# Optimization experiments

Hardware: AMD Instinct MI355X
Metric: run time of the kernel (lower is better)

The kernel has to match this reference:

```python
import jax, jax.numpy as jnp
import numpy as np

N_NODES = 50000
N_EDGES = 800000
N_FEAT = 128
HIDDEN = 256
BN_EPS = 1e-5


def setup_inputs() -> dict:
    key = jax.random.key(0)
    ks = jax.random.split(key, 8)
    x = jax.random.normal(ks[0], (N_NODES, N_FEAT), dtype=jnp.float32)
    edge_index = jax.random.randint(ks[1], (2, N_EDGES), 0, N_NODES, dtype=jnp.int64)
    # Xavier-uniform linear weights (as in weights_init), zero biases
    def xavier(k, fan_in, fan_out):
        lim = float(np.sqrt(6.0 / (fan_in + fan_out)))
        return jax.random.uniform(k, (fan_in, fan_out), jnp.float32, -lim, lim)
    return {
        "x": x,
        "edge_index": edge_index,
        "W1": xavier(ks[2], N_FEAT, HIDDEN),
        "b1": jnp.zeros((HIDDEN,), jnp.float32),
        "g1": jnp.ones((HIDDEN,), jnp.float32),
        "be1": jnp.zeros((HIDDEN,), jnp.float32),
        "W2": xavier(ks[3], HIDDEN, HIDDEN),
        "b2": jnp.zeros((HIDDEN,), jnp.float32),
        "g2": jnp.ones((HIDDEN,), jnp.float32),
        "be2": jnp.zeros((HIDDEN,), jnp.float32),
        "Wfc": xavier(ks[4], HIDDEN, HIDDEN),
        "bfc": jnp.zeros((HIDDEN,), jnp.float32),
    }


def gcn_conv(x, src, dst, deg_inv_sqrt, W, b):
    """PyG GCNConv: out_i = sum_{j->i} d_i^-1/2 d_j^-1/2 (x_j W) + b,
    with self-loops already appended to (src, dst)."""
    h = x @ W                                        # [N, out]
    norm = deg_inv_sqrt[src] * deg_inv_sqrt[dst]     # [E+N]
    msgs = h[src] * norm[:, None]                    # gather + scale
    out = jax.ops.segment_sum(msgs, dst, num_segments=x.shape[0])
    return out + b


def batch_norm(x, gamma, beta):
    # training-mode BatchNorm1d: batch stats over nodes, biased variance
    mean = jnp.mean(x, axis=0)
    var = jnp.mean(jnp.square(x - mean), axis=0)
    return (x - mean) * jax.lax.rsqrt(var + BN_EPS) * gamma + beta


def reference(x, edge_index, W1, b1, g1, be1, W2, b2, g2, be2, Wfc, bfc):
    n = x.shape[0]
    loop = jnp.arange(n, dtype=edge_index.dtype)
    src = jnp.concatenate([edge_index[0], loop])
    dst = jnp.concatenate([edge_index[1], loop])
    deg = jax.ops.segment_sum(jnp.ones_like(src, dtype=x.dtype), dst, num_segments=n)
    deg_inv_sqrt = jnp.where(deg > 0, jax.lax.rsqrt(jnp.maximum(deg, 1.0)), 0.0)

    h = gcn_conv(x, src, dst, deg_inv_sqrt, W1, b1)
    h = batch_norm(h, g1, be1)
    # dropout is identity in deterministic (eval) reference
    h = gcn_conv(h, src, dst, deg_inv_sqrt, W2, b2)
    h = batch_norm(h, g2, be2)
    return h @ Wfc + bfc
```

## Files before the change

### kernel.cpp

```cpp
#include <hip/hip_runtime.h>
#include <hip/hip_bf16.h>

#define NFEAT 128
#define HID 256
#define BN_EPS 1e-5f
#define NBIN 64

typedef __attribute__((ext_vector_type(8))) __bf16 bf16x8;
typedef __attribute__((ext_vector_type(4))) float f32x4;

static __device__ __forceinline__ float bflo(unsigned u) {
    union { unsigned x; float f; } c; c.x = u << 16; return c.f;
}
static __device__ __forceinline__ float bfhi(unsigned u) {
    union { unsigned x; float f; } c; c.x = u & 0xffff0000u; return c.f;
}

__global__ void k_count(const int* __restrict__ ei, int E, int* __restrict__ cnt,
                        int* __restrict__ rank) {
    int e = blockIdx.x * blockDim.x + threadIdx.x;
    if (e < E) rank[e] = atomicAdd(&cnt[ei[E + e]], 1);
}

__global__ void k_scan1(const int* __restrict__ cnt, int n, int* __restrict__ partial,
                        int* __restrict__ blk_total) {
    __shared__ int sh[256];
    int i = blockIdx.x * 256 + threadIdx.x;
    int v = (i < n) ? cnt[i] : 0;
    sh[threadIdx.x] = v;
    __syncthreads();
    for (int off = 1; off < 256; off <<= 1) {
        int x = (threadIdx.x >= off) ? sh[threadIdx.x - off] : 0;
        __syncthreads();
        sh[threadIdx.x] += x;
        __syncthreads();
    }
    if (i < n) partial[i] = sh[threadIdx.x] - v;
    if (threadIdx.x == 255) blk_total[blockIdx.x] = sh[255];
}

__global__ void k_finalize(const int* __restrict__ partial, const int* __restrict__ blk_total,
                           const int* __restrict__ cnt, int n, int nblk,
                           int* __restrict__ row_start, float* __restrict__ dinv) {
    __shared__ int sw[4];
    const int t = threadIdx.x;
    const int b = blockIdx.x;
    int v = (t < b && t < nblk) ? blk_total[t] : 0;
#pragma unroll
    for (int m = 1; m < 64; m <<= 1) v += __shfl_xor(v, m);
    if ((t & 63) == 0) sw[t >> 6] = v;
    __syncthreads();
    int pref = sw[0] + sw[1] + sw[2] + sw[3];
    int i = b * 256 + t;
    if (i < n) {
        row_start[i] = partial[i] + pref;
        dinv[i] = rsqrtf((float)(cnt[i] + 1));
    }
}

__global__ void k_fillcast(int fillBlocks, int castBlocks, const int* __restrict__ ei,
                           const int* __restrict__ rank, const int* __restrict__ row_start,
                           int E, int* __restrict__ col, const float* __restrict__ x,
                           const float* __restrict__ dinv, __hip_bfloat16* __restrict__ xs,
                           int n4, const float* __restrict__ W1,
                           __hip_bfloat16* __restrict__ Wt1) {
    const int bid = blockIdx.x;
    const int t = threadIdx.x;
    if (bid < fillBlocks) {
        int e = bid * 256 + t;
        if (e < E) {
            int d = ei[E + e];
            col[row_start[d] + rank[e]] = ei[e];
        }
    } else if (bid < fillBlocks + castBlocks) {
        int i = (bid - fillBlocks) * 256 + t;
        if (i < n4) {
            float d = dinv[i >> 5];
            float4 v = *(const float4*)(x + (size_t)i * 4);
            __hip_bfloat16* o = xs + (size_t)i * 4;
            o[0] = __float2bfloat16(v.x * d);
            o[1] = __float2bfloat16(v.y * d);
            o[2] = __float2bfloat16(v.z * d);
            o[3] = __float2bfloat16(v.w * d);
        }
    } else {
        int idx = (bid - fillBlocks - castBlocks) * 256 + t;
        int nn = idx & 255;
        int k = idx >> 8;
        Wt1[nn * 128 + k] = __float2bfloat16(W1[k * 256 + nn]);
    }
}

__global__ __launch_bounds__(256) void k_bnfoldW(const float* __restrict__ gs,
                                                 const float* __restrict__ g,
                                                 const float* __restrict__ be,
                                                 const float* __restrict__ b, float invN,
                                                 const float* __restrict__ W1,
                                                 const float* __restrict__ W2,
                                                 __hip_bfloat16* __restrict__ WfT,
                                                 float* __restrict__ uvec) {
    __shared__ float shs[256], shb[256];
    const int c = threadIdx.x;
    float s = 0.f, q = 0.f;
    for (int r = 0; r < NBIN; r++) {
        s += gs[r * 512 + c];
        q += gs[r * 512 + 256 + c];
    }
    float mean = s * invN;
    float var = q * invN - mean * mean;
    float scl = rsqrtf(var + BN_EPS) * g[c];
    shs[c] = scl;
    shb[c] = (b[c] - mean) * scl + be[c];
    __syncthreads();
    if (blockIdx.x < 128) {
        int k = blockIdx.x;
        float acc = 0.f;
        for (int m = 0; m < 256; m++) acc += W1[k * 256 + m] * shs[m] * W2[m * 256 + c];
        WfT[(size_t)c * 128 + k] = __float2bfloat16(acc);
    } else {
        float acc = 0.f;
        for (int m = 0; m < 256; m++) acc += W2[m * 256 + c] * shb[m];
        uvec[c] = acc;
    }
}

__global__ __launch_bounds__(256) void k_fold2(const float* __restrict__ gs,
                                               const float* __restrict__ g,
                                               const float* __restrict__ be, float invN,
                                               const float* __restrict__ Wfc,
                                               const float* __restrict__ bfc,
                                               __hip_bfloat16* __restrict__ Wtf,
                                               float* __restrict__ bias2) {
    __shared__ float shs[256], sho[256];
    const int c = threadIdx.x;
    float s = 0.f, q = 0.f;
    for (int r = 0; r < NBIN; r++) {
        s += gs[r * 512 + c];
        q += gs[r * 512 + 256 + c];
    }
    float mean = s * invN;
    float var = q * invN - mean * mean;
    float scl = rsqrtf(var + BN_EPS) * g[c];
    shs[c] = scl;
    sho[c] = (0.f - mean) * scl + be[c];
    __syncthreads();
    if (blockIdx.x < 256) {
        int k = blockIdx.x;
        Wtf[(size_t)c * 256 + k] = __float2bfloat16(Wfc[k * 256 + c] * shs[k]);
    } else {
        float acc = bfc[c];
        for (int m = 0; m < 256; m++) acc += sho[m] * Wfc[m * 256 + c];
        bias2[c] = acc;
    }
}

template <bool SCALE>
__global__ __launch_bounds__(256) void k_spmm(const __hip_bfloat16* __restrict__ Hs,
                                              const int* __restrict__ rs,
                                              const int* __restrict__ rc,
                                              const int* __restrict__ col,
                                              const float* __restrict__ dinv,
                                              __hip_bfloat16* __restrict__ out,
                                              float* __restrict__ rv, int N) {
    const int wid = blockIdx.x * 4 + (threadIdx.x >> 6);
    if (wid >= N) return;
    const int lane = threadIdx.x & 63;
    const int ch = lane * 2;
    const int s = rs[wid];
    const int deg = rc[wid];
    const float di = dinv[wid];

    unsigned u0 = *(const unsigned*)(Hs + (size_t)wid * 128 + ch);
    float a0, a1, dsum = 0.f;
    if constexpr (SCALE) { a0 = di * bflo(u0); a1 = di * bfhi(u0); }
    else { a0 = bflo(u0); a1 = bfhi(u0); }

    int e = 0;
    for (; e + 8 <= deg; e += 8) {
        int idx[8];
#pragma unroll
        for (int j = 0; j < 8; j++) idx[j] = col[s + e + j];
        float dj[8];
#pragma unroll
        for (int j = 0; j < 8; j++) dj[j] = dinv[idx[j]];
        unsigned u[8];
#pragma unroll
        for (int j = 0; j < 8; j++) u[j] = *(const unsigned*)(Hs + (size_t)idx[j] * 128 + ch);
#pragma unroll
        for (int j = 0; j < 8; j++) {
            if constexpr (SCALE) { a0 += dj[j] * bflo(u[j]); a1 += dj[j] * bfhi(u[j]); }
            else { a0 += bflo(u[j]); a1 += bfhi(u[j]); dsum += dj[j]; }
        }
    }
    for (; e < deg; e++) {
        int i0 = col[s + e];
        float d0 = dinv[i0];
        unsigned uu = *(const unsigned*)(Hs + (size_t)i0 * 128 + ch);
        if constexpr (SCALE) { a0 += d0 * bflo(uu); a1 += d0 * bfhi(uu); }
        else { a0 += bflo(uu); a1 += bfhi(uu); dsum += d0; }
    }
    union { unsigned w; unsigned short us[2]; } o;
    __hip_bfloat16 b0 = __float2bfloat16(di * a0); o.us[0] = *(unsigned short*)&b0;
    __hip_bfloat16 b1 = __float2bfloat16(di * a1); o.us[1] = *(unsigned short*)&b1;
    *(unsigned*)(out + (size_t)wid * 128 + ch) = o.w;
    if (!SCALE && rv && lane == 0) rv[wid] = di * (di + dsum);
}

template <int K, bool STATS>
__global__ __launch_bounds__(256, 4) void k_gemm2(const __hip_bfloat16* __restrict__ A,
                                                  const __hip_bfloat16* __restrict__ Bt,
                                                  const float* __restrict__ bias,
                                                  __hip_bfloat16* __restrict__ outb,
                                                  float* __restrict__ outf,
                                                  float* __restrict__ gs,
                                                  const float* __restrict__ rvec,
                                                  const float* __restrict__ uvec, int M) {
    constexpr int NC = K / 64;
    constexpr int LDR = 72;
    __shared__ __align__(16) unsigned short Bs[2 * 128 * LDR];
    float* sred = (float*)Bs;
    float* qred = sred + 512;

    const int t = threadIdx.x;
    const int wv = t >> 6;
    const int lane = t & 63;
    const int mlane = lane & 15;
    const int quad = lane >> 4;
    const int m0 = blockIdx.x * 128;
    const int n0 = blockIdx.y * 128;
    const int arow0 = m0 + wv * 32 + mlane;

    auto stage = [&](int c, int buf) {
#pragma unroll
        for (int i = 0; i < 4; i++) {
            int idx = t + i * 256;
            int row = idx >> 3;
            int c4 = idx & 7;
            uint4 v = *(const uint4*)(Bt + (size_t)(n0 + row) * K + c * 64 + c4 * 8);
            *(uint4*)(Bs + buf * (128 * LDR) + row * LDR + c4 * 8) = v;
        }
    };
    auto loadA = [&](int c, bf16x8 (&dst)[2][2]) {
#pragma unroll
        for (int mt = 0; mt < 2; mt++)
#pragma unroll
            for (int ks = 0; ks < 2; ks++)
                dst[mt][ks] = *(const bf16x8*)(A + (size_t)(arow0 + mt * 16) * K + c * 64 +
                                               ks * 32 + quad * 8);
    };

    f32x4 acc[2][8];
#pragma unroll
    for (int mt = 0; mt < 2; mt++)
#pragma unroll
        for (int i = 0; i < 8; i++) acc[mt][i] = (f32x4){0.f, 0.f, 0.f, 0.f};

    bf16x8 aP[2][2], aQ[2][2];
    loadA(0, aP);
    stage(0, 0);

    auto mmachunk = [&](int c, bf16x8 (&ac)[2][2]) {
        const unsigned short* base = Bs + (c & 1) * (128 * LDR);
#pragma unroll
        for (int nt = 0; nt < 8; nt++) {
            const unsigned short* bp = base + (nt * 16 + mlane) * LDR + quad * 8;
#pragma unroll
            for (int ks = 0; ks < 2; ks++) {
                bf16x8 b = *(const bf16x8*)(bp + ks * 32);
                acc[0][nt] = __builtin_amdgcn_mfma_f32_16x16x32_bf16(ac[0][ks], b, acc[0][nt], 0, 0, 0);
                acc[1][nt] = __builtin_amdgcn_mfma_f32_16x16x32_bf16(ac[1][ks], b, acc[1][nt], 0, 0, 0);
            }
        }
    };

#pragma unroll
    for (int c = 0; c < NC; c++) {
        __syncthreads();
        if (c + 1 < NC) {
            stage(c + 1, (c + 1) & 1);
            if ((c & 1) == 0) loadA(c + 1, aQ); else loadA(c + 1, aP);
        }
        if ((c & 1) == 0) mmachunk(c, aP); else mmachunk(c, aQ);
    }

    float rv[2][4] = {{0.f, 0.f, 0.f, 0.f}, {0.f, 0.f, 0.f, 0.f}};
    if (rvec) {
#pragma unroll
        for (int mt = 0; mt < 2; mt++)
#pragma unroll
            for (int r = 0; r < 4; r++) {
                int row = m0 + wv * 32 + mt * 16 + quad * 4 + r;
                if (row < M) rv[mt][r] = rvec[row];
            }
    }
    float sp[8], qp[8];
#pragma unroll
    for (int nt = 0; nt < 8; nt++) {
        int colx = n0 + nt * 16 + mlane;
        float bv = bias[colx];
        float uvn = uvec ? uvec[colx] : 0.f;
        float s = 0.f, q = 0.f;
#pragma unroll
        for (int mt = 0; mt < 2; mt++)
#pragma unroll
            for (int r = 0; r < 4; r++) {
                int row = m0 + wv * 32 + mt * 16 + quad * 4 + r;
                if (row < M) {
                    float h = acc[mt][nt][r] + bv + rv[mt][r] * uvn;
                    if (outb) outb[(size_t)row * HID + colx] = __float2bfloat16(h);
                    if (outf) outf[(size_t)row * HID + colx] = h;
                    s += h;
                    q += h * h;
                }
            }
        sp[nt] = s;
        qp[nt] = q;
    }
    if constexpr (STATS) {
#pragma unroll
        for (int nt = 0; nt < 8; nt++) {
            sp[nt] += __shfl_xor(sp[nt], 16);
            sp[nt] += __shfl_xor(sp[nt], 32);
            qp[nt] += __shfl_xor(qp[nt], 16);
            qp[nt] += __shfl_xor(qp[nt], 32);
        }
        __syncthreads();
        if (quad == 0) {
#pragma unroll
            for (int nt = 0; nt < 8; nt++) {
                sred[wv * 128 + nt * 16 + mlane] = sp[nt];
                qred[wv * 128 + nt * 16 + mlane] = qp[nt];
            }
        }
        __syncthreads();
        if (t < 128) {
            float ss = sred[t] + sred[128 + t] + sred[256 + t] + sred[384 + t];
            float qq = qred[t] + qred[128 + t] + qred[256 + t] + qred[384 + t];
            float* bin = gs + (blockIdx.x & (NBIN - 1)) * 512;
            atomicAdd(&bin[n0 + t], ss);
            atomicAdd(&bin[256 + n0 + t], qq);
        }
    }
}

extern "C" void kernel_launch(void* const* d_in, const int* in_sizes, int n_in, void* d_out,
                              int out_size, void* d_ws, size_t ws_size, hipStream_t stream) {
    const float* x = (const float*)d_in[0];
    const int* ei = (const int*)d_in[1];
    const float* W1 = (const float*)d_in[2];
    const float* b1 = (const float*)d_in[3];
    const float* g1 = (const float*)d_in[4];
    const float* be1 = (const float*)d_in[5];
    const float* W2 = (const float*)d_in[6];
    const float* b2 = (const float*)d_in[7];
    const float* g2 = (const float*)d_in[8];
    const float* be2 = (const float*)d_in[9];
    const float* Wfc = (const float*)d_in[10];
    const float* bfc = (const float*)d_in[11];
    float* out = (float*)d_out;

    const int N = in_sizes[0] / NFEAT;
    const int E = in_sizes[1] / 2;
    const float invN = 1.0f / (float)N;

    char* ws = (char*)d_ws;
    size_t off = 0;
    auto alloc = [&](size_t bytes) -> void* {
        void* p = ws + off;
        off += (bytes + 255) & ~(size_t)255;
        return p;
    };
    int* row_cnt = (int*)alloc((size_t)N * 4);
    float* gs1 = (float*)alloc((size_t)NBIN * 512 * 4);
    float* gs2 = (float*)alloc((size_t)NBIN * 512 * 4);
    size_t zero_bytes = off;
    int* partial = (int*)alloc((size_t)N * 4);
    int* row_start = (int*)alloc((size_t)N * 4);
    int* blk = (int*)alloc(256 * 4);
    float* dinv = (float*)alloc((size_t)N * 4);
    int* rank = (int*)alloc((size_t)E * 4);
    int* col_idx = (int*)alloc((size_t)E * 4);
    float* uvec = (float*)alloc(256 * 4);
    float* bias2 = (float*)alloc(256 * 4);
    float* rvec = (float*)alloc((size_t)(N + 128) * 4);
    __hip_bfloat16* Wt1 = (__hip_bfloat16*)alloc(256 * 128 * 2);
    __hip_bfloat16* Wtf = (__hip_bfloat16*)alloc(256 * 256 * 2);
    __hip_bfloat16* WfT = (__hip_bfloat16*)alloc(256 * 128 * 2);
    __hip_bfloat16* xs = (__hip_bfloat16*)alloc((size_t)(N + 128) * NFEAT * 2);
    __hip_bfloat16* aggX = (__hip_bfloat16*)alloc((size_t)(N + 128) * NFEAT * 2);
    __hip_bfloat16* h2 = (__hip_bfloat16*)alloc((size_t)(N + 128) * HID * 2);
    __hip_bfloat16* t2 = xs;

    hipMemsetAsync(row_cnt, 0, zero_bytes, stream);

    const int nblk = (N + 255) / 256;
    const int fillBlocks = (E + 255) / 256;
    const int castBlocks = (N * NFEAT / 4 + 255) / 256;

    k_count<<<fillBlocks, 256, 0, stream>>>(ei, E, row_cnt, rank);
    k_scan1<<<nblk, 256, 0, stream>>>(row_cnt, N, partial, blk);
    k_finalize<<<nblk, 256, 0, stream>>>(partial, blk, row_cnt, N, nblk, row_start, dinv);
    k_fillcast<<<fillBlocks + castBlocks + 128, 256, 0, stream>>>(
        fillBlocks, castBlocks, ei, rank, row_start, E, col_idx, x, dinv, xs,
        N * NFEAT / 4, W1, Wt1);

    const int sg = (N + 3) / 4;
    dim3 gg((N + 127) / 128, 2);

    k_spmm<false><<<sg, 256, 0, stream>>>(xs, row_start, row_cnt, col_idx, dinv, aggX, rvec, N);
    k_spmm<true><<<sg, 256, 0, stream>>>(aggX, row_start, row_cnt, col_idx, dinv, t2, nullptr, N);
    k_gemm2<NFEAT, true><<<gg, 256, 0, stream>>>(aggX, Wt1, b1, nullptr, nullptr, gs1,
                                                 nullptr, nullptr, N);
    k_bnfoldW<<<129, 256, 0, stream>>>(gs1, g1, be1, b1, invN, W1, W2, WfT, uvec);
    k_gemm2<NFEAT, true><<<gg, 256, 0, stream>>>(t2, WfT, b2, h2, nullptr, gs2, rvec, uvec, N);
    k_fold2<<<257, 256, 0, stream>>>(gs2, g2, be2, invN, Wfc, bfc, Wtf, bias2);
    k_gemm2<HID, false><<<gg, 256, 0, stream>>>(h2, Wtf, bias2, nullptr, out, nullptr,
                                                nullptr, nullptr, N);
}
```

Before: 314.3 us.

## Compute BatchNorm statistics via Gram matrices and fold all layers into one GEMM

Instead of running per-layer GEMMs that materialize hidden activations just to collect BatchNorm mean and variance, the code now builds 128x128 Gram matrices and column sums of the aggregated inputs. It derives the BN statistics analytically from these through the weight matrices. Both BN layers and the final linear layer are then folded into a single 128-to-256 weight, so only one large GEMM over nodes remains. This removes two full-size GEMMs and the bf16 hidden buffer. In exchange it adds several small reduction kernels, and the E[h^2]-mean^2 variance computed from bf16 Gram sums may lose precision.

```diff
diff --git a/kernel.cpp b/kernel.cpp
--- a/kernel.cpp
+++ b/kernel.cpp
@@ -4,7 +4,9 @@
 #define NFEAT 128
 #define HID 256
 #define BN_EPS 1e-5f
-#define NBIN 64
+#define GR 64
+#define GLDW 72
+#define GB 128
 
 typedef __attribute__((ext_vector_type(8))) __bf16 bf16x8;
 typedef __attribute__((ext_vector_type(4))) float f32x4;
@@ -58,12 +60,11 @@
     }
 }
 
-__global__ void k_fillcast(int fillBlocks, int castBlocks, const int* __restrict__ ei,
+__global__ void k_fillcast(int fillBlocks, const int* __restrict__ ei,
                            const int* __restrict__ rank, const int* __restrict__ row_start,
                            int E, int* __restrict__ col, const float* __restrict__ x,
                            const float* __restrict__ dinv, __hip_bfloat16* __restrict__ xs,
-                           int n4, const float* __restrict__ W1,
-                           __hip_bfloat16* __restrict__ Wt1) {
+                           int n4) {
     const int bid = blockIdx.x;
     const int t = threadIdx.x;
     if (bid < fillBlocks) {
@@ -72,7 +73,7 @@
             int d = ei[E + e];
             col[row_start[d] + rank[e]] = ei[e];
         }
-    } else if (bid < fillBlocks + castBlocks) {
+    } else {
         int i = (bid - fillBlocks) * 256 + t;
         if (i < n4) {
             float d = dinv[i >> 5];
@@ -83,74 +84,6 @@
             o[2] = __float2bfloat16(v.z * d);
             o[3] = __float2bfloat16(v.w * d);
         }
-    } else {
-        int idx = (bid - fillBlocks - castBlocks) * 256 + t;
-        int nn = idx & 255;
-        int k = idx >> 8;
-        Wt1[nn * 128 + k] = __float2bfloat16(W1[k * 256 + nn]);
-    }
-}
-
-__global__ __launch_bounds__(256) void k_bnfoldW(const float* __restrict__ gs,
-                                                 const float* __restrict__ g,
-                                                 const float* __restrict__ be,
-                                                 const float* __restrict__ b, float invN,
-                                                 const float* __restrict__ W1,
-                                                 const float* __restrict__ W2,
-                                                 __hip_bfloat16* __restrict__ WfT,
-                                                 float* __restrict__ uvec) {
-    __shared__ float shs[256], shb[256];
-    const int c = threadIdx.x;
-    float s = 0.f, q = 0.f;
-    for (int r = 0; r < NBIN; r++) {
-        s += gs[r * 512 + c];
-        q += gs[r * 512 + 256 + c];
-    }
-    float mean = s * invN;
-    float var = q * invN - mean * mean;
-    float scl = rsqrtf(var + BN_EPS) * g[c];
-    shs[c] = scl;
-    shb[c] = (b[c] - mean) * scl + be[c];
-    __syncthreads();
-    if (blockIdx.x < 128) {
-        int k = blockIdx.x;
-        float acc = 0.f;
-        for (int m = 0; m < 256; m++) acc += W1[k * 256 + m] * shs[m] * W2[m * 256 + c];
-        WfT[(size_t)c * 128 + k] = __float2bfloat16(acc);
-    } else {
-        float acc = 0.f;
-        for (int m = 0; m < 256; m++) acc += W2[m * 256 + c] * shb[m];
-        uvec[c] = acc;
-    }
-}
-
-__global__ __launch_bounds__(256) void k_fold2(const float* __restrict__ gs,
-                                               const float* __restrict__ g,
-                                               const float* __restrict__ be, float invN,
-                                               const float* __restrict__ Wfc,
-                                               const float* __restrict__ bfc,
-                                               __hip_bfloat16* __restrict__ Wtf,
-                                               float* __restrict__ bias2) {
-    __shared__ float shs[256], sho[256];
-    const int c = threadIdx.x;
-    float s = 0.f, q = 0.f;
-    for (int r = 0; r < NBIN; r++) {
-        s += gs[r * 512 + c];
-        q += gs[r * 512 + 256 + c];
-    }
-    float mean = s * invN;
-    float var = q * invN - mean * mean;
-    float scl = rsqrtf(var + BN_EPS) * g[c];
-    shs[c] = scl;
-    sho[c] = (0.f - mean) * scl + be[c];
-    __syncthreads();
-    if (blockIdx.x < 256) {
-        int k = blockIdx.x;
-        Wtf[(size_t)c * 256 + k] = __float2bfloat16(Wfc[k * 256 + c] * shs[k]);
-    } else {
-        float acc = bfc[c];
-        for (int m = 0; m < 256; m++) acc += sho[m] * Wfc[m * 256 + c];
-        bias2[c] = acc;
     }
 }
 
@@ -206,20 +139,289 @@
     if (!SCALE && rv && lane == 0) rv[wid] = di * (di + dsum);
 }
 
-template <int K, bool STATS>
+__global__ __launch_bounds__(256) void k_gram(const __hip_bfloat16* __restrict__ X1,
+                                              const __hip_bfloat16* __restrict__ X2,
+                                              const float* __restrict__ rvec,
+                                              float* __restrict__ Gp1, float* __restrict__ Gp2,
+                                              float* __restrict__ vp1, float* __restrict__ vp2,
+                                              int N) {
+    __shared__ __align__(16) unsigned short XT[128 * GLDW];
+    __shared__ float sdr[GR];
+    __shared__ float sred[256];
+    const int t = threadIdx.x;
+    const int wv = t >> 6;
+    const int lane = t & 63;
+    const int mlane = lane & 15;
+    const int quad = lane >> 4;
+    const bool r1 = (int)blockIdx.x >= GB;
+    const int bid = r1 ? blockIdx.x - GB : blockIdx.x;
+    const __hip_bfloat16* X = r1 ? X2 : X1;
+    float* Gp = (r1 ? Gp2 : Gp1) + (size_t)bid * 16384;
+    float* vpb = r1 ? (vp2 + (size_t)bid * 260) : (vp1 + (size_t)bid * 128);
+
+    f32x4 acc[2][8];
+#pragma unroll
+    for (int mt = 0; mt < 2; mt++)
+#pragma unroll
+        for (int i = 0; i < 8; i++) acc[mt][i] = (f32x4){0.f, 0.f, 0.f, 0.f};
+    float csum = 0.f, c2s = 0.f, srs = 0.f, sr2s = 0.f;
+
+    const int nc = (N + GR - 1) / GR;
+    for (int chk = bid; chk < nc; chk += GB) {
+        const int row0 = chk * GR;
+        __syncthreads();
+#pragma unroll
+        for (int i = 0; i < 4; i++) {
+            int idx = t + i * 256;
+            int k = idx & (GR - 1);
+            int g = idx >> 6;
+            int row = row0 + k;
+            uint4 v = (row < N) ? *(const uint4*)(X + (size_t)row * 128 + g * 8)
+                                : make_uint4(0u, 0u, 0u, 0u);
+            const unsigned short* pv = (const unsigned short*)&v;
+#pragma unroll
+            for (int c = 0; c < 8; c++) XT[(g * 8 + c) * GLDW + k] = pv[c];
+        }
+        if (r1 && t < GR) {
+            int row = row0 + t;
+            sdr[t] = (row < N) ? rvec[row] : 0.f;
+        }
+        __syncthreads();
+        {
+            int cch = t & 127, h = t >> 7;
+            float cs = 0.f, cc = 0.f;
+#pragma unroll
+            for (int k = 0; k < GR / 2; k++) {
+                int kk = h * (GR / 2) + k;
+                float xv = bflo((unsigned)XT[cch * GLDW + kk]);
+                cs += xv;
+                if (r1) cc += xv * sdr[kk];
+            }
+            csum += cs;
+            c2s += cc;
+            if (r1 && t < GR) { float r = sdr[t]; srs += r; sr2s += r * r; }
+        }
+#pragma unroll
+        for (int ks = 0; ks < 2; ks++) {
+            bf16x8 af[2];
+#pragma unroll
+            for (int mt = 0; mt < 2; mt++)
+                af[mt] = *(const bf16x8*)(XT + (wv * 32 + mt * 16 + mlane) * GLDW +
+                                          ks * 32 + quad * 8);
+#pragma unroll
+            for (int nt = 0; nt < 8; nt++) {
+                bf16x8 bfr = *(const bf16x8*)(XT + (nt * 16 + mlane) * GLDW + ks * 32 + quad * 8);
+                acc[0][nt] = __builtin_amdgcn_mfma_f32_16x16x32_bf16(af[0], bfr, acc[0][nt], 0, 0, 0);
+                acc[1][nt] = __builtin_amdgcn_mfma_f32_16x16x32_bf16(af[1], bfr, acc[1][nt], 0, 0, 0);
+            }
+        }
+    }
+#pragma unroll
+    for (int mt = 0; mt < 2; mt++)
+#pragma unroll
+        for (int nt = 0; nt < 8; nt++)
+#pragma unroll
+            for (int r = 0; r < 4; r++)
+                Gp[(wv * 32 + mt * 16 + quad * 4 + r) * 128 + nt * 16 + mlane] = acc[mt][nt][r];
+    sred[t] = csum;
+    __syncthreads();
+    if (t < 128) vpb[t] = sred[t] + sred[t + 128];
+    if (r1) {
+        __syncthreads();
+        sred[t] = c2s;
+        __syncthreads();
+        if (t < 128) vpb[128 + t] = sred[t] + sred[t + 128];
+        if (t < 64) {
+            float a = srs, b = sr2s;
+#pragma unroll
+            for (int m = 1; m < 64; m <<= 1) { a += __shfl_xor(a, m); b += __shfl_xor(b, m); }
+            if (t == 0) { vpb[256] = a; vpb[257] = b; }
+        }
+    }
+}
+
+__global__ __launch_bounds__(256) void k_gfold(const float* __restrict__ Gp1,
+                                               const float* __restrict__ Gp2,
+                                               const float* __restrict__ vp1,
+                                               const float* __restrict__ vp2,
+                                               float* __restrict__ G1, float* __restrict__ G2,
+                                               float* __restrict__ svec) {
+    const int b = blockIdx.x, t = threadIdx.x;
+    if (b < 64) {
+        int e = b * 256 + t;
+        float s = 0.f;
+        for (int p = 0; p < GB; p++) s += Gp1[(size_t)p * 16384 + e];
+        G1[e] = s;
+    } else if (b < 128) {
+        int e = (b - 64) * 256 + t;
+        float s = 0.f;
+        for (int p = 0; p < GB; p++) s += Gp2[(size_t)p * 16384 + e];
+        G2[e] = s;
+    } else {
+        if (t < 128) {
+            float s = 0.f;
+            for (int p = 0; p < GB; p++) s += vp1[(size_t)p * 128 + t];
+            svec[t] = s;
+        } else {
+            int c = t - 128;
+            float s = 0.f;
+            for (int p = 0; p < GB; p++) s += vp2[(size_t)p * 260 + c];
+            svec[128 + c] = s;
+        }
+        __syncthreads();
+        if (t < 128) {
+            float s = 0.f;
+            for (int p = 0; p < GB; p++) s += vp2[(size_t)p * 260 + 128 + t];
+            svec[256 + t] = s;
+        } else if (t == 128) {
+            float s = 0.f;
+            for (int p = 0; p < GB; p++) s += vp2[(size_t)p * 260 + 256];
+            svec[384] = s;
+        } else if (t == 129) {
+            float s = 0.f;
+            for (int p = 0; p < GB; p++) s += vp2[(size_t)p * 260 + 257];
+            svec[385] = s;
+        }
+    }
+}
+
+__global__ __launch_bounds__(128) void k_bnstat1(const float* __restrict__ G1,
+                                                 const float* __restrict__ svec,
+                                                 const float* __restrict__ W1,
+                                                 const float* __restrict__ b1,
+                                                 const float* __restrict__ g1,
+                                                 const float* __restrict__ be1, float invN,
+                                                 float fN, float* __restrict__ sc1,
+                                                 float* __restrict__ bv1) {
+    __shared__ float shw[128], s1[128], s2[128];
+    const int c = blockIdx.x, t = threadIdx.x;
+    shw[t] = W1[t * 256 + c];
+    __syncthreads();
+    const float* gr = G1 + t * 128;
+    float v = 0.f;
+    for (int b = 0; b < 128; b++) v += gr[b] * shw[b];
+    s1[t] = v * shw[t];
+    s2[t] = svec[t] * shw[t];
+    __syncthreads();
+    for (int off = 64; off; off >>= 1) {
+        if (t < off) { s1[t] += s1[t + off]; s2[t] += s2[t + off]; }
+        __syncthreads();
+    }
+    if (t == 0) {
+        float bb = b1[c], mdot = s2[0], vdot = s1[0];
+        float mean = (mdot + fN * bb) * invN;
+        float eh2 = (vdot + 2.f * bb * mdot + fN * bb * bb) * invN;
+        float var = eh2 - mean * mean;
+        float s = rsqrtf(var + BN_EPS) * g1[c];
+        sc1[c] = s;
+        bv1[c] = (bb - mean) * s + be1[c];
+    }
+}
+
+__global__ __launch_bounds__(256) void k_bnfoldW(const float* __restrict__ sc1,
+                                                 const float* __restrict__ bv1,
+                                                 const float* __restrict__ W1,
+                                                 const float* __restrict__ W2,
+                                                 __hip_bfloat16* __restrict__ WfT,
+                                                 float* __restrict__ uvec) {
+    __shared__ float shs[256], shb[256];
+    const int c = threadIdx.x;
+    shs[c] = sc1[c];
+    shb[c] = bv1[c];
+    __syncthreads();
+    if (blockIdx.x < 128) {
+        int k = blockIdx.x;
+        float acc = 0.f;
+        for (int m = 0; m < 256; m++) acc += W1[k * 256 + m] * shs[m] * W2[m * 256 + c];
+        WfT[(size_t)c * 128 + k] = __float2bfloat16(acc);
+    } else {
+        float acc = 0.f;
+        for (int m = 0; m < 256; m++) acc += W2[m * 256 + c] * shb[m];
+        uvec[c] = acc;
+    }
+}
+
+__global__ __launch_bounds__(128) void k_bnstat2(const float* __restrict__ G2,
+                                                 const float* __restrict__ svec,
+                                                 const __hip_bfloat16* __restrict__ WfT,
+                                                 const float* __restrict__ uvec,
+                                                 const float* __restrict__ b2,
+                                                 const float* __restrict__ g2,
+                                                 const float* __restrict__ be2, float invN,
+                                                 float fN, float* __restrict__ sc2,
+                                                 float* __restrict__ ofb2) {
+    __shared__ float shw[128], s1[128], s2[128], s3[128];
+    const int c = blockIdx.x, t = threadIdx.x;
+    shw[t] = __bfloat162float(WfT[(size_t)c * 128 + t]);
+    __syncthreads();
+    const float* gr = G2 + t * 128;
+    float v = 0.f;
+    for (int b = 0; b < 128; b++) v += gr[b] * shw[b];
+    s1[t] = v * shw[t];
+    s2[t] = svec[128 + t] * shw[t];
+    s3[t] = svec[256 + t] * shw[t];
+    __syncthreads();
+    for (int off = 64; off; off >>= 1) {
+        if (t < off) { s1[t] += s1[t + off]; s2[t] += s2[t + off]; s3[t] += s3[t + off]; }
+        __syncthreads();
+    }
+    if (t == 0) {
+        float bb = b2[c], u = uvec[c];
+        float vdot = s1[0], mdot = s2[0], cdot = s3[0];
+        float Sr = svec[384], Sr2 = svec[385];
+        float mean = (mdot + Sr * u + fN * bb) * invN;
+        float eh2 = (vdot + 2.f * u * cdot + 2.f * bb * mdot + Sr2 * u * u +
+                     2.f * bb * u * Sr + fN * bb * bb) * invN;
+        float var = eh2 - mean * mean;
+        float s = rsqrtf(var + BN_EPS) * g2[c];
+        sc2[c] = s;
+        ofb2[c] = (bb - mean) * s + be2[c];
+    }
+}
+
+__global__ __launch_bounds__(256) void k_foldbig(const float* __restrict__ sc2,
+                                                 const float* __restrict__ ofb2,
+                                                 const float* __restrict__ uvec,
+                                                 const float* __restrict__ Wfc,
+                                                 const float* __restrict__ bfc,
+                                                 const __hip_bfloat16* __restrict__ WfT,
+                                                 __hip_bfloat16* __restrict__ WbigT,
+                                                 float* __restrict__ vvec,
+                                                 float* __restrict__ cvec) {
+    __shared__ float sh[256];
+    const int t = threadIdx.x;
+    if (blockIdx.x < 256) {
+        int n = blockIdx.x;
+        sh[t] = sc2[t] * Wfc[t * 256 + n];
+        __syncthreads();
+        if (t < 128) {
+            float acc = 0.f;
+            for (int m = 0; m < 256; m++)
+                acc += __bfloat162float(WfT[(size_t)m * 128 + t]) * sh[m];
+            WbigT[(size_t)n * 128 + t] = __float2bfloat16(acc);
+        }
+    } else {
+        float av = 0.f, ac = bfc[t];
+        for (int m = 0; m < 256; m++) {
+            float w = Wfc[m * 256 + t];
+            av += uvec[m] * sc2[m] * w;
+            ac += ofb2[m] * w;
+        }
+        vvec[t] = av;
+        cvec[t] = ac;
+    }
+}
+
+template <int K>
 __global__ __launch_bounds__(256, 4) void k_gemm2(const __hip_bfloat16* __restrict__ A,
                                                   const __hip_bfloat16* __restrict__ Bt,
                                                   const float* __restrict__ bias,
-                                                  __hip_bfloat16* __restrict__ outb,
                                                   float* __restrict__ outf,
-                                                  float* __restrict__ gs,
                                                   const float* __restrict__ rvec,
                                                   const float* __restrict__ uvec, int M) {
     constexpr int NC = K / 64;
     constexpr int LDR = 72;
     __shared__ __align__(16) unsigned short Bs[2 * 128 * LDR];
-    float* sred = (float*)Bs;
-    float* qred = sred + 512;
 
     const int t = threadIdx.x;
     const int wv = t >> 6;
@@ -284,62 +486,25 @@
     }
 
     float rv[2][4] = {{0.f, 0.f, 0.f, 0.f}, {0.f, 0.f, 0.f, 0.f}};
-    if (rvec) {
-#pragma unroll
-        for (int mt = 0; mt < 2; mt++)
-#pragma unroll
-            for (int r = 0; r < 4; r++) {
-                int row = m0 + wv * 32 + mt * 16 + quad * 4 + r;
-                if (row < M) rv[mt][r] = rvec[row];
-            }
-    }
-    float sp[8], qp[8];
+#pragma unroll
+    for (int mt = 0; mt < 2; mt++)
+#pragma unroll
+        for (int r = 0; r < 4; r++) {
+            int row = m0 + wv * 32 + mt * 16 + quad * 4 + r;
+            if (row < M) rv[mt][r] = rvec[row];
+        }
 #pragma unroll
     for (int nt = 0; nt < 8; nt++) {
         int colx = n0 + nt * 16 + mlane;
         float bv = bias[colx];
-        float uvn = uvec ? uvec[colx] : 0.f;
-        float s = 0.f, q = 0.f;
+        float uvn = uvec[colx];
 #pragma unroll
         for (int mt = 0; mt < 2; mt++)
 #pragma unroll
             for (int r = 0; r < 4; r++) {
                 int row = m0 + wv * 32 + mt * 16 + quad * 4 + r;
-                if (row < M) {
-                    float h = acc[mt][nt][r] + bv + rv[mt][r] * uvn;
-                    if (outb) outb[(size_t)row * HID + colx] = __float2bfloat16(h);
-                    if (outf) outf[(size_t)row * HID + colx] = h;
-                    s += h;
-                    q += h * h;
-                }
+                if (row < M) outf[(size_t)row * HID + colx] = acc[mt][nt][r] + bv + rv[mt][r] * uvn;
             }
-        sp[nt] = s;
-        qp[nt] = q;
-    }
-    if constexpr (STATS) {
-#pragma unroll
-        for (int nt = 0; nt < 8; nt++) {
-            sp[nt] += __shfl_xor(sp[nt], 16);
-            sp[nt] += __shfl_xor(sp[nt], 32);
-            qp[nt] += __shfl_xor(qp[nt], 16);
-            qp[nt] += __shfl_xor(qp[nt], 32);
-        }
-        __syncthreads();
-        if (quad == 0) {
-#pragma unroll
-            for (int nt = 0; nt < 8; nt++) {
-                sred[wv * 128 + nt * 16 + mlane] = sp[nt];
-                qred[wv * 128 + nt * 16 + mlane] = qp[nt];
-            }
-        }
-        __syncthreads();
-        if (t < 128) {
-            float ss = sred[t] + sred[128 + t] + sred[256 + t] + sred[384 + t];
-            float qq = qred[t] + qred[128 + t] + qred[256 + t] + qred[384 + t];
-            float* bin = gs + (blockIdx.x & (NBIN - 1)) * 512;
-            atomicAdd(&bin[n0 + t], ss);
-            atomicAdd(&bin[256 + n0 + t], qq);
-        }
     }
 }
 
@@ -362,6 +527,7 @@
     const int N = in_sizes[0] / NFEAT;
     const int E = in_sizes[1] / 2;
     const float invN = 1.0f / (float)N;
+    const float fN = (float)N;
 
     char* ws = (char*)d_ws;
     size_t off = 0;
@@ -371,8 +537,6 @@
         return p;
     };
     int* row_cnt = (int*)alloc((size_t)N * 4);
-    float* gs1 = (float*)alloc((size_t)NBIN * 512 * 4);
-    float* gs2 = (float*)alloc((size_t)NBIN * 512 * 4);
     size_t zero_bytes = off;
     int* partial = (int*)alloc((size_t)N * 4);
     int* row_start = (int*)alloc((size_t)N * 4);
@@ -380,15 +544,25 @@
     float* dinv = (float*)alloc((size_t)N * 4);
     int* rank = (int*)alloc((size_t)E * 4);
     int* col_idx = (int*)alloc((size_t)E * 4);
+    float* rvec = (float*)alloc((size_t)(N + 128) * 4);
+    float* Gp1 = (float*)alloc((size_t)GB * 16384 * 4);
+    float* Gp2 = (float*)alloc((size_t)GB * 16384 * 4);
+    float* vp1 = (float*)alloc((size_t)GB * 128 * 4);
+    float* vp2 = (float*)alloc((size_t)GB * 260 * 4);
+    float* G1 = (float*)alloc(16384 * 4);
+    float* G2 = (float*)alloc(16384 * 4);
+    float* svec = (float*)alloc(400 * 4);
+    float* sc1 = (float*)alloc(256 * 4);
+    float* bv1 = (float*)alloc(256 * 4);
     float* uvec = (float*)alloc(256 * 4);
-    float* bias2 = (float*)alloc(256 * 4);
-    float* rvec = (float*)alloc((size_t)(N + 128) * 4);
-    __hip_bfloat16* Wt1 = (__hip_bfloat16*)alloc(256 * 128 * 2);
-    __hip_bfloat16* Wtf = (__hip_bfloat16*)alloc(256 * 256 * 2);
+    float* sc2 = (float*)alloc(256 * 4);
+    float* ofb2 = (float*)alloc(256 * 4);
+    float* vvec = (float*)alloc(256 * 4);
+    float* cvec = (float*)alloc(256 * 4);
     __hip_bfloat16* WfT = (__hip_bfloat16*)alloc(256 * 128 * 2);
+    __hip_bfloat16* WbigT = (__hip_bfloat16*)alloc(256 * 128 * 2);
     __hip_bfloat16* xs = (__hip_bfloat16*)alloc((size_t)(N + 128) * NFEAT * 2);
     __hip_bfloat16* aggX = (__hip_bfloat16*)alloc((size_t)(N + 128) * NFEAT * 2);
-    __hip_bfloat16* h2 = (__hip_bfloat16*)alloc((size_t)(N + 128) * HID * 2);
     __hip_bfloat16* t2 = xs;
 
     hipMemsetAsync(row_cnt, 0, zero_bytes, stream);
@@ -400,20 +574,20 @@
     k_count<<<fillBlocks, 256, 0, stream>>>(ei, E, row_cnt, rank);
     k_scan1<<<nblk, 256, 0, stream>>>(row_cnt, N, partial, blk);
     k_finalize<<<nblk, 256, 0, stream>>>(partial, blk, row_cnt, N, nblk, row_start, dinv);
-    k_fillcast<<<fillBlocks + castBlocks + 128, 256, 0, stream>>>(
-        fillBlocks, castBlocks, ei, rank, row_start, E, col_idx, x, dinv, xs,
-        N * NFEAT / 4, W1, Wt1);
+    k_fillcast<<<fillBlocks + castBlocks, 256, 0, stream>>>(fillBlocks, ei, rank, row_start, E,
+                                                            col_idx, x, dinv, xs, N * NFEAT / 4);
 
     const int sg = (N + 3) / 4;
-    dim3 gg((N + 127) / 128, 2);
-
     k_spmm<false><<<sg, 256, 0, stream>>>(xs, row_start, row_cnt, col_idx, dinv, aggX, rvec, N);
     k_spmm<true><<<sg, 256, 0, stream>>>(aggX, row_start, row_cnt, col_idx, dinv, t2, nullptr, N);
-    k_gemm2<NFEAT, true><<<gg, 256, 0, stream>>>(aggX, Wt1, b1, nullptr, nullptr, gs1,
-                                                 nullptr, nullptr, N);
-    k_bnfoldW<<<129, 256, 0, stream>>>(gs1, g1, be1, b1, invN, W1, W2, WfT, uvec);
-    k_gemm2<NFEAT, true><<<gg, 256, 0, stream>>>(t2, WfT, b2, h2, nullptr, gs2, rvec, uvec, N);
-    k_fold2<<<257, 256, 0, stream>>>(gs2, g2, be2, invN, Wfc, bfc, Wtf, bias2);
-    k_gemm2<HID, false><<<gg, 256, 0, stream>>>(h2, Wtf, bias2, nullptr, out, nullptr,
-                                                nullptr, nullptr, N);
-}
+
+    k_gram<<<2 * GB, 256, 0, stream>>>(aggX, t2, rvec, Gp1, Gp2, vp1, vp2, N);
+    k_gfold<<<129, 256, 0, stream>>>(Gp1, Gp2, vp1, vp2, G1, G2, svec);
+    k_bnstat1<<<256, 128, 0, stream>>>(G1, svec, W1, b1, g1, be1, invN, fN, sc1, bv1);
+    k_bnfoldW<<<129, 256, 0, stream>>>(sc1, bv1, W1, W2, WfT, uvec);
+    k_bnstat2<<<256, 128, 0, stream>>>(G2, svec, WfT, uvec, b2, g2, be2, invN, fN, sc2, ofb2);
+    k_foldbig<<<257, 256, 0, stream>>>(sc2, ofb2, uvec, Wfc, bfc, WfT, WbigT, vvec, cvec);
+
+    dim3 gg((N + 127) / 128, 2);
+    k_gemm2<NFEAT><<<gg, 256, 0, stream>>>(t2, WbigT, cvec, out, rvec, vvec, N);
+}
```

New measurement: 323.6 us. 2.9% more time.
